# Optimization experiments

Hardware: AMD Instinct MI355X
Metric: run time of the kernel (lower is better)

The kernel has to match this reference:

```python
import jax, jax.numpy as jnp
import numpy as np

N_NODES = 100000


def sage_conv(x, src, dst, W_l, b_l, W_r):
    # PyG SAGEConv (aggr='mean'): out = lin_l(mean_{j->i} x_j) + lin_r(x_i)
    # lin_l has bias, lin_r does not.
    msgs = x[src]                                             # [E, d_in] irregular gather
    summed = jax.ops.segment_sum(msgs, dst, num_segments=N_NODES)
    deg = jax.ops.segment_sum(jnp.ones((src.shape[0],), x.dtype), dst,
                              num_segments=N_NODES)
    mean = summed / jnp.maximum(deg, 1.0)[:, None]            # [N, d_in]
    return mean @ W_l.T + b_l + x @ W_r.T                     # [N, d_out]


def setup_inputs() -> dict:
    key = jax.random.key(0)
    ks = jax.random.split(key, 8)
    input_dim, hidden_dim, output_dim = 64, 128, 64
    E = 1600000
    x = jax.random.normal(ks[0], (N_NODES, input_dim), dtype=jnp.float32)
    edge_index = jax.random.randint(ks[1], (2, E), 0, N_NODES, dtype=jnp.int64)

    def glorot(k, shape):
        lim = (6.0 / (shape[0] + shape[1])) ** 0.5
        return jax.random.uniform(k, shape, jnp.float32, -lim, lim)

    W1_l = glorot(ks[2], (hidden_dim, input_dim))
    b1 = jnp.zeros((hidden_dim,), jnp.float32)
    W1_r = glorot(ks[3], (hidden_dim, input_dim))
    W2_l = glorot(ks[4], (output_dim, hidden_dim))
    b2 = jnp.zeros((output_dim,), jnp.float32)
    W2_r = glorot(ks[5], (output_dim, hidden_dim))
    return {"x": x, "edge_index": edge_index,
            "W1_l": W1_l, "b1": b1, "W1_r": W1_r,
            "W2_l": W2_l, "b2": b2, "W2_r": W2_r}


def reference(x, edge_index, W1_l, b1, W1_r, W2_l, b2, W2_r):
    src, dst = edge_index[0], edge_index[1]
    h = jax.nn.relu(sage_conv(x, src, dst, W1_l, b1, W1_r))
    h = jax.nn.relu(sage_conv(h, src, dst, W2_l, b2, W2_r))
    # Original module computes norm(x) and dropout(x) but discards the results,
    # so the returned value is just the second ReLU output.
    return h
```

## Files before the change

kernel.cpp:

```cpp
#include <hip/hip_runtime.h>
#include <hip/hip_bf16.h>


#define NODE_DIM0 64
#define NPBK 256
#define MAXB 512
#define CAPB 5120
#define EPB  4096
#define NSL  16

__device__ inline unsigned short f2bf(float f) {
    unsigned u = __float_as_uint(f);
    return (unsigned short)((u + 0x7fffu + ((u >> 16) & 1u)) >> 16);
}


__global__ __launch_bounds__(256) void bucket_scatter(const int* __restrict__ src,
                                                      const int* __restrict__ dst,
                                                      int* __restrict__ gcur,
                                                      unsigned* __restrict__ pairs, int E) {
    __shared__ int hist[MAXB];
    __shared__ int incl[MAXB];
    __shared__ int exoff[MAXB];
    __shared__ int cur[MAXB];
    __shared__ int chunkBase[MAXB];
    __shared__ unsigned staged[EPB];
    __shared__ unsigned short sbkt[EPB];
    const int t = threadIdx.x;
    const int base = blockIdx.x * EPB;
    int cnt = E - base; if (cnt > EPB) cnt = EPB;

    hist[t] = 0; hist[t + 256] = 0;
    __syncthreads();

    int myS[16], myD[16];
#pragma unroll
    for (int it = 0; it < 16; ++it) {
        int e = base + it * 256 + t;
        if (e < E) {
            myS[it] = src[e];
            myD[it] = dst[e];
            atomicAdd(&hist[myD[it] >> 8], 1);
        } else {
            myD[it] = -1;
        }
    }
    __syncthreads();

    incl[t] = hist[t]; incl[t + 256] = hist[t + 256];
    __syncthreads();
    for (int o = 1; o < MAXB; o <<= 1) {
        int a0 = (t >= o) ? incl[t - o] : 0;
        int a1 = (t + 256 >= o) ? incl[t + 256 - o] : 0;
        __syncthreads();
        incl[t] += a0; incl[t + 256] += a1;
        __syncthreads();
    }
    exoff[t] = incl[t] - hist[t];
    exoff[t + 256] = incl[t + 256] - hist[t + 256];
    cur[t] = 0; cur[t + 256] = 0;
    chunkBase[t] = (hist[t] > 0) ? atomicAdd(&gcur[t], hist[t]) : 0;
    chunkBase[t + 256] = (hist[t + 256] > 0) ? atomicAdd(&gcur[t + 256], hist[t + 256]) : 0;
    __syncthreads();

#pragma unroll
    for (int it = 0; it < 16; ++it) {
        if (myD[it] >= 0) {
            int b = myD[it] >> 8;
            int p = exoff[b] + atomicAdd(&cur[b], 1);
            staged[p] = ((unsigned)(myD[it] & (NPBK - 1)) << 17) | (unsigned)myS[it];
            sbkt[p] = (unsigned short)b;
        }
    }
    __syncthreads();

    for (int p = t; p < cnt; p += 256) {
        int b = sbkt[p];
        int g = chunkBase[b] + (p - exoff[b]);
        if (g < CAPB) pairs[(size_t)b * CAPB + g] = staged[p];
    }
}


__global__ __launch_bounds__(256) void bucket_csr(const unsigned* __restrict__ pairs,
                                                  const int* __restrict__ gcur,
                                                  int* __restrict__ startA,
                                                  int* __restrict__ degA,
                                                  int* __restrict__ esrc, int N) {
    __shared__ int ldeg[NPBK * NSL];
    __shared__ int lcur[NPBK * NSL];
    __shared__ int lsrc[CAPB];
    __shared__ int wsum[256];
    const int b = blockIdx.x;
    const int t = threadIdx.x;
    int cnt = gcur[b]; if (cnt > CAPB) cnt = CAPB;

    for (int i = t; i < NPBK * NSL; i += 256) ldeg[i] = 0;
    __syncthreads();

    const unsigned* reg = pairs + (size_t)b * CAPB;
    for (int i = t; i < cnt; i += 256) {
        unsigned w = reg[i];
        atomicAdd(&ldeg[((w >> 17) << 4) | ((w & 0x1FFFFu) >> 13)], 1);
    }
    __syncthreads();

    const int base = t * NSL;
    int run = 0, loc[NSL];
#pragma unroll
    for (int k = 0; k < NSL; ++k) { loc[k] = run; run += ldeg[base + k]; }
    wsum[t] = run;
    __syncthreads();
    for (int o = 1; o < 256; o <<= 1) {
        int add = (t >= o) ? wsum[t - o] : 0;
        __syncthreads();
        wsum[t] += add;
        __syncthreads();
    }
    const int excl = wsum[t] - run;
#pragma unroll
    for (int k = 0; k < NSL; ++k) lcur[base + k] = excl + loc[k];
    const int node0 = b * NPBK;
    if (node0 + t < N) { startA[node0 + t] = b * CAPB + excl; degA[node0 + t] = run; }
    __syncthreads();

    for (int i = t; i < cnt; i += 256) {
        unsigned w = reg[i];
        int key = ((w >> 17) << 4) | ((w & 0x1FFFFu) >> 13);
        int pos = atomicAdd(&lcur[key], 1);
        lsrc[pos] = (int)(w & 0x1FFFFu);
    }
    __syncthreads();

    int* out = esrc + (size_t)b * CAPB;
    for (int i = t; i < cnt; i += 256) out[i] = lsrc[i];
}


__global__ void cast_bf(const float* __restrict__ in, unsigned short* __restrict__ out, int n4) {
    int i = blockIdx.x * 256 + threadIdx.x;
    if (i < n4) {
        float4 v = ((const float4*)in)[i];
        ushort4 o;
        o.x = f2bf(v.x); o.y = f2bf(v.y); o.z = f2bf(v.z); o.w = f2bf(v.w);
        ((ushort4*)out)[i] = o;
    }
}

__global__ void cast_weights(const float* __restrict__ a, const float* __restrict__ b,
                             const float* __restrict__ c, const float* __restrict__ d,
                             unsigned short* __restrict__ oa, unsigned short* __restrict__ ob,
                             unsigned short* __restrict__ oc, unsigned short* __restrict__ od) {
    int i = blockIdx.x * 256 + threadIdx.x;
    if (i < 8192) {
        oa[i] = f2bf(a[i]); ob[i] = f2bf(b[i]);
        oc[i] = f2bf(c[i]); od[i] = f2bf(d[i]);
    }
}


template <int MODE>
__global__ __launch_bounds__(256) void gather64(const unsigned short* __restrict__ feat,
                                                const int* __restrict__ startA,
                                                const int* __restrict__ degA,
                                                const int* __restrict__ esrc,
                                                const unsigned short* __restrict__ sdata,
                                                unsigned short* __restrict__ meanOut,
                                                float* __restrict__ outF, int n) {
    const int w = (blockIdx.x * 256 + threadIdx.x) >> 3;
    const int fl = threadIdx.x & 7;
    if (w >= n) return;
    const int s0 = startA[w], dg = degA[w];
    float acc[8] = {0.f, 0.f, 0.f, 0.f, 0.f, 0.f, 0.f, 0.f};
    const int* ep = esrc + s0;
    int e = 0;
    for (; e + 8 <= dg; e += 8) {
        int s_[8];
#pragma unroll
        for (int k = 0; k < 8; ++k) s_[k] = ep[e + k];
        uint4 u[8];
#pragma unroll
        for (int k = 0; k < 8; ++k)
            u[k] = *(const uint4*)(feat + (size_t)s_[k] * 64 + fl * 8);
#pragma unroll
        for (int k = 0; k < 8; ++k) {
            acc[0] += __uint_as_float(u[k].x << 16);
            acc[1] += __uint_as_float(u[k].x & 0xffff0000u);
            acc[2] += __uint_as_float(u[k].y << 16);
            acc[3] += __uint_as_float(u[k].y & 0xffff0000u);
            acc[4] += __uint_as_float(u[k].z << 16);
            acc[5] += __uint_as_float(u[k].z & 0xffff0000u);
            acc[6] += __uint_as_float(u[k].w << 16);
            acc[7] += __uint_as_float(u[k].w & 0xffff0000u);
        }
    }
    for (; e < dg; ++e) {
        uint4 u = *(const uint4*)(feat + (size_t)ep[e] * 64 + fl * 8);
        acc[0] += __uint_as_float(u.x << 16);
        acc[1] += __uint_as_float(u.x & 0xffff0000u);
        acc[2] += __uint_as_float(u.y << 16);
        acc[3] += __uint_as_float(u.y & 0xffff0000u);
        acc[4] += __uint_as_float(u.z << 16);
        acc[5] += __uint_as_float(u.z & 0xffff0000u);
        acc[6] += __uint_as_float(u.w << 16);
        acc[7] += __uint_as_float(u.w & 0xffff0000u);
    }
    const float inv = 1.0f / fmaxf((float)dg, 1.0f);
    if (MODE == 0) {
        unsigned us[8];
#pragma unroll
        for (int q = 0; q < 8; ++q) us[q] = f2bf(acc[q] * inv);
        uint4 o4;
        o4.x = us[0] | (us[1] << 16);
        o4.y = us[2] | (us[3] << 16);
        o4.z = us[4] | (us[5] << 16);
        o4.w = us[6] | (us[7] << 16);
        *(uint4*)(meanOut + (size_t)w * 64 + fl * 8) = o4;
    } else {
        uint4 us = *(const uint4*)(sdata + (size_t)w * 64 + fl * 8);
        float sv8[8];
        sv8[0] = __uint_as_float(us.x << 16);
        sv8[1] = __uint_as_float(us.x & 0xffff0000u);
        sv8[2] = __uint_as_float(us.y << 16);
        sv8[3] = __uint_as_float(us.y & 0xffff0000u);
        sv8[4] = __uint_as_float(us.z << 16);
        sv8[5] = __uint_as_float(us.z & 0xffff0000u);
        sv8[6] = __uint_as_float(us.w << 16);
        sv8[7] = __uint_as_float(us.w & 0xffff0000u);
        float4 o0, o1;
        o0.x = fmaxf(acc[0] * inv + sv8[0], 0.f);
        o0.y = fmaxf(acc[1] * inv + sv8[1], 0.f);
        o0.z = fmaxf(acc[2] * inv + sv8[2], 0.f);
        o0.w = fmaxf(acc[3] * inv + sv8[3], 0.f);
        o1.x = fmaxf(acc[4] * inv + sv8[4], 0.f);
        o1.y = fmaxf(acc[5] * inv + sv8[5], 0.f);
        o1.z = fmaxf(acc[6] * inv + sv8[6], 0.f);
        o1.w = fmaxf(acc[7] * inv + sv8[7], 0.f);
        *(float4*)(outF + (size_t)w * 64 + fl * 8)     = o0;
        *(float4*)(outF + (size_t)w * 64 + fl * 8 + 4) = o1;
    }
}


__global__ __launch_bounds__(256) void fused_l12(const unsigned short* __restrict__ meanb,
                                                 const unsigned short* __restrict__ selfb,
                                                 const unsigned short* __restrict__ W1l,
                                                 const float* __restrict__ b1,
                                                 const unsigned short* __restrict__ W1r,
                                                 const unsigned short* __restrict__ W2l,
                                                 const float* __restrict__ b2,
                                                 const unsigned short* __restrict__ W2r,
                                                 unsigned short* __restrict__ zout,
                                                 unsigned short* __restrict__ sout, int n) {
    using bf16x8 = __attribute__((ext_vector_type(8))) short;
    using f32x4  = __attribute__((ext_vector_type(4))) float;
    constexpr int LDW = 136;
    __shared__ unsigned short h1t[16 * LDW];
    const int wv   = threadIdx.x >> 6;
    const int lane = threadIdx.x & 63;
    const int row16 = lane & 15;
    const int quad  = lane >> 4;

    bf16x8 bl1[2][2], br1[2][2];
    float bv1[2];
#pragma unroll
    for (int r = 0; r < 2; ++r) {
        int nc = (wv * 2 + r) * 16 + row16;
#pragma unroll
        for (int kk = 0; kk < 2; ++kk) {
            bl1[r][kk] = *(const bf16x8*)(W1l + (size_t)nc * 64 + kk * 32 + quad * 8);
            br1[r][kk] = *(const bf16x8*)(W1r + (size_t)nc * 64 + kk * 32 + quad * 8);
        }
        bv1[r] = b1[nc];
    }
    const int nc2 = wv * 16 + row16;
    bf16x8 bl2[4], br2[4];
#pragma unroll
    for (int kk = 0; kk < 4; ++kk) {
        bl2[kk] = *(const bf16x8*)(W2l + (size_t)nc2 * 128 + kk * 32 + quad * 8);
        br2[kk] = *(const bf16x8*)(W2r + (size_t)nc2 * 128 + kk * 32 + quad * 8);
    }
    const float bv2 = b2[nc2];

    const int mtiles = n / 16;
    for (int mt = blockIdx.x; mt < mtiles; mt += gridDim.x) {
        const int m = mt * 16 + row16;
        bf16x8 am[2], as2[2];
#pragma unroll
        for (int kk = 0; kk < 2; ++kk) {
            am[kk]  = *(const bf16x8*)(meanb + (size_t)m * 64 + kk * 32 + quad * 8);
            as2[kk] = *(const bf16x8*)(selfb + (size_t)m * 64 + kk * 32 + quad * 8);
        }
#pragma unroll
        for (int r = 0; r < 2; ++r) {
            f32x4 acc = {0.f, 0.f, 0.f, 0.f};
#pragma unroll
            for (int kk = 0; kk < 2; ++kk)
                acc = __builtin_amdgcn_mfma_f32_16x16x32_bf16(am[kk], bl1[r][kk], acc, 0, 0, 0);
#pragma unroll
            for (int kk = 0; kk < 2; ++kk)
                acc = __builtin_amdgcn_mfma_f32_16x16x32_bf16(as2[kk], br1[r][kk], acc, 0, 0, 0);
            const int nc = (wv * 2 + r) * 16 + row16;
#pragma unroll
            for (int i = 0; i < 4; ++i)
                h1t[(quad * 4 + i) * LDW + nc] = f2bf(fmaxf(acc[i] + bv1[r], 0.f));
        }
        __syncthreads();
        bf16x8 a2[4];
#pragma unroll
        for (int kk = 0; kk < 4; ++kk)
            a2[kk] = *(const bf16x8*)(h1t + row16 * LDW + kk * 32 + quad * 8);
        f32x4 accz = {0.f, 0.f, 0.f, 0.f};
        f32x4 accs = {0.f, 0.f, 0.f, 0.f};
#pragma unroll
        for (int kk = 0; kk < 4; ++kk) {
            accz = __builtin_amdgcn_mfma_f32_16x16x32_bf16(a2[kk], bl2[kk], accz, 0, 0, 0);
            accs = __builtin_amdgcn_mfma_f32_16x16x32_bf16(a2[kk], br2[kk], accs, 0, 0, 0);
        }
        const int rowb = mt * 16 + quad * 4;
#pragma unroll
        for (int i = 0; i < 4; ++i) {
            zout[(size_t)(rowb + i) * 64 + nc2] = f2bf(accz[i]);
            sout[(size_t)(rowb + i) * 64 + nc2] = f2bf(accs[i] + bv2);
        }
        __syncthreads();
    }
}


static inline char* align_up(char* p, size_t a) {
    return (char*)(((uintptr_t)p + a - 1) & ~(uintptr_t)(a - 1));
}

extern "C" void kernel_launch(void* const* d_in, const int* in_sizes, int n_in,
                              void* d_out, int out_size, void* d_ws, size_t ws_size,
                              hipStream_t stream) {
    const float* x   = (const float*)d_in[0];
    const int*   ei  = (const int*)d_in[1];
    const float* W1l = (const float*)d_in[2];
    const float* b1  = (const float*)d_in[3];
    const float* W1r = (const float*)d_in[4];
    const float* W2l = (const float*)d_in[5];
    const float* b2  = (const float*)d_in[6];
    const float* W2r = (const float*)d_in[7];
    float* out = (float*)d_out;

    const int N = in_sizes[0] / NODE_DIM0;
    const int E = in_sizes[1] / 2;
    const int* src = ei;
    const int* dst = ei + E;
    const int nbuck = (N + NPBK - 1) / NPBK;

    char* p = (char*)d_ws;
    int* gcur   = (int*)p; p += (size_t)MAXB * 4;          p = align_up(p, 16);
    int* startA = (int*)p; p += (size_t)N * 4;             p = align_up(p, 16);
    int* degA   = (int*)p; p += (size_t)N * 4;             p = align_up(p, 16);
    int* esrc   = (int*)p; p += (size_t)nbuck * CAPB * 4;  p = align_up(p, 16);
    unsigned short* xbf   = (unsigned short*)p; p += (size_t)N * 64 * 2;
    unsigned short* scr2  = (unsigned short*)p; p += (size_t)N * 128 * 2;
    unsigned short* wl1bf = (unsigned short*)p; p += (size_t)128 * 64 * 2;
    unsigned short* wr1bf = (unsigned short*)p; p += (size_t)128 * 64 * 2;
    unsigned short* wl2bf = (unsigned short*)p; p += (size_t)64 * 128 * 2;
    unsigned short* wr2bf = (unsigned short*)p; p += (size_t)64 * 128 * 2;
    unsigned short* meanbf = (unsigned short*)p; p += (size_t)N * 64 * 2;

    unsigned* pairs = (unsigned*)scr2;
    unsigned short* zbf = scr2;
    unsigned short* sbf = scr2 + (size_t)N * 64;

    hipMemsetAsync(gcur, 0, (size_t)MAXB * 4, stream);
    bucket_scatter<<<(E + EPB - 1) / EPB, 256, 0, stream>>>(src, dst, gcur, pairs, E);
    bucket_csr<<<nbuck, 256, 0, stream>>>(pairs, gcur, startA, degA, esrc, N);

    cast_bf<<<(N * 64 / 4 + 255) / 256, 256, 0, stream>>>(x, xbf, N * 64 / 4);
    cast_weights<<<32, 256, 0, stream>>>(W1l, W1r, W2l, W2r, wl1bf, wr1bf, wl2bf, wr2bf);

    gather64<0><<<(N * 8 + 255) / 256, 256, 0, stream>>>(xbf, startA, degA, esrc, nullptr, meanbf, nullptr, N);

    fused_l12<<<1024, 256, 0, stream>>>(meanbf, xbf, wl1bf, b1, wr1bf,
                                        wl2bf, b2, wr2bf, zbf, sbf, N);

    gather64<1><<<(N * 8 + 255) / 256, 256, 0, stream>>>(zbf, startA, degA, esrc, sbf, nullptr, out, N);
}
```

Baseline: 224.5 us.

## Drop LDS staging in bucket build, fold memset and weight casts into kernels

The bucket scatter now uses the rank returned by its shared-memory histogram atomic to write pairs straight to global memory, which removes the prefix scan and the staged LDS copy. The CSR kernel likewise keeps each element's rank in registers and scatters directly into esrc without an LDS buffer. The gcur memset moves into the cast kernel, and the weight cast kernel is removed, with fused_l12 converting fp32 weights to bf16 as it loads them. This cuts two launches and several block barriers, but the global writes become less coalesced. Each of the 1024 fused blocks also repeats the weight conversion.

```diff
diff --git a/kernel.cpp b/kernel.cpp
--- a/kernel.cpp
+++ b/kernel.cpp
@@ -20,64 +20,41 @@
                                                       int* __restrict__ gcur,
                                                       unsigned* __restrict__ pairs, int E) {
     __shared__ int hist[MAXB];
-    __shared__ int incl[MAXB];
-    __shared__ int exoff[MAXB];
-    __shared__ int cur[MAXB];
     __shared__ int chunkBase[MAXB];
-    __shared__ unsigned staged[EPB];
-    __shared__ unsigned short sbkt[EPB];
     const int t = threadIdx.x;
     const int base = blockIdx.x * EPB;
-    int cnt = E - base; if (cnt > EPB) cnt = EPB;
 
     hist[t] = 0; hist[t + 256] = 0;
     __syncthreads();
 
-    int myS[16], myD[16];
+    int myS[16], myD[16], myR[16];
 #pragma unroll
     for (int it = 0; it < 16; ++it) {
         int e = base + it * 256 + t;
         if (e < E) {
             myS[it] = src[e];
             myD[it] = dst[e];
-            atomicAdd(&hist[myD[it] >> 8], 1);
+            myR[it] = atomicAdd(&hist[myD[it] >> 8], 1);
         } else {
             myD[it] = -1;
         }
     }
     __syncthreads();
 
-    incl[t] = hist[t]; incl[t + 256] = hist[t + 256];
-    __syncthreads();
-    for (int o = 1; o < MAXB; o <<= 1) {
-        int a0 = (t >= o) ? incl[t - o] : 0;
-        int a1 = (t + 256 >= o) ? incl[t + 256 - o] : 0;
-        __syncthreads();
-        incl[t] += a0; incl[t + 256] += a1;
-        __syncthreads();
-    }
-    exoff[t] = incl[t] - hist[t];
-    exoff[t + 256] = incl[t + 256] - hist[t + 256];
-    cur[t] = 0; cur[t + 256] = 0;
-    chunkBase[t] = (hist[t] > 0) ? atomicAdd(&gcur[t], hist[t]) : 0;
-    chunkBase[t + 256] = (hist[t + 256] > 0) ? atomicAdd(&gcur[t + 256], hist[t + 256]) : 0;
+    int h0 = hist[t], h1 = hist[t + 256];
+    chunkBase[t]       = (h0 > 0) ? atomicAdd(&gcur[t], h0) : 0;
+    chunkBase[t + 256] = (h1 > 0) ? atomicAdd(&gcur[t + 256], h1) : 0;
     __syncthreads();
 
 #pragma unroll
     for (int it = 0; it < 16; ++it) {
         if (myD[it] >= 0) {
             int b = myD[it] >> 8;
-            int p = exoff[b] + atomicAdd(&cur[b], 1);
-            staged[p] = ((unsigned)(myD[it] & (NPBK - 1)) << 17) | (unsigned)myS[it];
-            sbkt[p] = (unsigned short)b;
-        }
-    }
-    __syncthreads();
-
-    for (int p = t; p < cnt; p += 256) {
-        int b = sbkt[p];
-        int g = chunkBase[b] + (p - exoff[b]);
-        if (g < CAPB) pairs[(size_t)b * CAPB + g] = staged[p];
+            int g = chunkBase[b] + myR[it];
+            if (g < CAPB)
+                pairs[(size_t)b * CAPB + g] =
+                    ((unsigned)(myD[it] & (NPBK - 1)) << 17) | (unsigned)myS[it];
+        }
     }
 }
 
@@ -88,8 +65,7 @@
                                                   int* __restrict__ degA,
                                                   int* __restrict__ esrc, int N) {
     __shared__ int ldeg[NPBK * NSL];
-    __shared__ int lcur[NPBK * NSL];
-    __shared__ int lsrc[CAPB];
+    __shared__ int koff[NPBK * NSL];
     __shared__ int wsum[256];
     const int b = blockIdx.x;
     const int t = threadIdx.x;
@@ -99,16 +75,22 @@
     __syncthreads();
 
     const unsigned* reg = pairs + (size_t)b * CAPB;
+    unsigned myW[20]; int myR[20], myK[20];
+    int nn = 0;
     for (int i = t; i < cnt; i += 256) {
         unsigned w = reg[i];
-        atomicAdd(&ldeg[((w >> 17) << 4) | ((w & 0x1FFFFu) >> 13)], 1);
-    }
-    __syncthreads();
-
-    const int base = t * NSL;
+        int key = (int)((w >> 17) << 4) | (int)((w & 0x1FFFFu) >> 13);
+        myW[nn] = w;
+        myK[nn] = key;
+        myR[nn] = atomicAdd(&ldeg[key], 1);
+        ++nn;
+    }
+    __syncthreads();
+
+    const int kbase = t * NSL;
     int run = 0, loc[NSL];
 #pragma unroll
-    for (int k = 0; k < NSL; ++k) { loc[k] = run; run += ldeg[base + k]; }
+    for (int k = 0; k < NSL; ++k) { loc[k] = run; run += ldeg[kbase + k]; }
     wsum[t] = run;
     __syncthreads();
     for (int o = 1; o < 256; o <<= 1) {
@@ -119,42 +101,27 @@
     }
     const int excl = wsum[t] - run;
 #pragma unroll
-    for (int k = 0; k < NSL; ++k) lcur[base + k] = excl + loc[k];
+    for (int k = 0; k < NSL; ++k) koff[kbase + k] = excl + loc[k];
     const int node0 = b * NPBK;
     if (node0 + t < N) { startA[node0 + t] = b * CAPB + excl; degA[node0 + t] = run; }
     __syncthreads();
 
-    for (int i = t; i < cnt; i += 256) {
-        unsigned w = reg[i];
-        int key = ((w >> 17) << 4) | ((w & 0x1FFFFu) >> 13);
-        int pos = atomicAdd(&lcur[key], 1);
-        lsrc[pos] = (int)(w & 0x1FFFFu);
-    }
-    __syncthreads();
-
-    int* out = esrc + (size_t)b * CAPB;
-    for (int i = t; i < cnt; i += 256) out[i] = lsrc[i];
-}
-
-
-__global__ void cast_bf(const float* __restrict__ in, unsigned short* __restrict__ out, int n4) {
+    int* outp = esrc + (size_t)b * CAPB;
+    for (int k = 0; k < nn; ++k)
+        outp[koff[myK[k]] + myR[k]] = (int)(myW[k] & 0x1FFFFu);
+}
+
+
+__global__ void cast_bf(const float* __restrict__ in, unsigned short* __restrict__ out,
+                        int n4, int* __restrict__ gcur) {
+    if (blockIdx.x == 0)
+        for (int j = threadIdx.x; j < MAXB; j += 256) gcur[j] = 0;
     int i = blockIdx.x * 256 + threadIdx.x;
     if (i < n4) {
         float4 v = ((const float4*)in)[i];
         ushort4 o;
         o.x = f2bf(v.x); o.y = f2bf(v.y); o.z = f2bf(v.z); o.w = f2bf(v.w);
         ((ushort4*)out)[i] = o;
-    }
-}
-
-__global__ void cast_weights(const float* __restrict__ a, const float* __restrict__ b,
-                             const float* __restrict__ c, const float* __restrict__ d,
-                             unsigned short* __restrict__ oa, unsigned short* __restrict__ ob,
-                             unsigned short* __restrict__ oc, unsigned short* __restrict__ od) {
-    int i = blockIdx.x * 256 + threadIdx.x;
-    if (i < 8192) {
-        oa[i] = f2bf(a[i]); ob[i] = f2bf(b[i]);
-        oc[i] = f2bf(c[i]); od[i] = f2bf(d[i]);
     }
 }
 
@@ -244,12 +211,12 @@
 
 __global__ __launch_bounds__(256) void fused_l12(const unsigned short* __restrict__ meanb,
                                                  const unsigned short* __restrict__ selfb,
-                                                 const unsigned short* __restrict__ W1l,
+                                                 const float* __restrict__ W1l,
                                                  const float* __restrict__ b1,
-                                                 const unsigned short* __restrict__ W1r,
-                                                 const unsigned short* __restrict__ W2l,
+                                                 const float* __restrict__ W1r,
+                                                 const float* __restrict__ W2l,
                                                  const float* __restrict__ b2,
-                                                 const unsigned short* __restrict__ W2r,
+                                                 const float* __restrict__ W2r,
                                                  unsigned short* __restrict__ zout,
                                                  unsigned short* __restrict__ sout, int n) {
     using bf16x8 = __attribute__((ext_vector_type(8))) short;
@@ -268,8 +235,13 @@
         int nc = (wv * 2 + r) * 16 + row16;
 #pragma unroll
         for (int kk = 0; kk < 2; ++kk) {
-            bl1[r][kk] = *(const bf16x8*)(W1l + (size_t)nc * 64 + kk * 32 + quad * 8);
-            br1[r][kk] = *(const bf16x8*)(W1r + (size_t)nc * 64 + kk * 32 + quad * 8);
+            const float* pl = W1l + (size_t)nc * 64 + kk * 32 + quad * 8;
+            const float* pr = W1r + (size_t)nc * 64 + kk * 32 + quad * 8;
+#pragma unroll
+            for (int i = 0; i < 8; ++i) {
+                bl1[r][kk][i] = (short)f2bf(pl[i]);
+                br1[r][kk][i] = (short)f2bf(pr[i]);
+            }
         }
         bv1[r] = b1[nc];
     }
@@ -277,8 +249,13 @@
     bf16x8 bl2[4], br2[4];
 #pragma unroll
     for (int kk = 0; kk < 4; ++kk) {
-        bl2[kk] = *(const bf16x8*)(W2l + (size_t)nc2 * 128 + kk * 32 + quad * 8);
-        br2[kk] = *(const bf16x8*)(W2r + (size_t)nc2 * 128 + kk * 32 + quad * 8);
+        const float* pl = W2l + (size_t)nc2 * 128 + kk * 32 + quad * 8;
+        const float* pr = W2r + (size_t)nc2 * 128 + kk * 32 + quad * 8;
+#pragma unroll
+        for (int i = 0; i < 8; ++i) {
+            bl2[kk][i] = (short)f2bf(pl[i]);
+            br2[kk][i] = (short)f2bf(pr[i]);
+        }
     }
     const float bv2 = b2[nc2];
 
@@ -358,27 +335,21 @@
     int* esrc   = (int*)p; p += (size_t)nbuck * CAPB * 4;  p = align_up(p, 16);
     unsigned short* xbf   = (unsigned short*)p; p += (size_t)N * 64 * 2;
     unsigned short* scr2  = (unsigned short*)p; p += (size_t)N * 128 * 2;
-    unsigned short* wl1bf = (unsigned short*)p; p += (size_t)128 * 64 * 2;
-    unsigned short* wr1bf = (unsigned short*)p; p += (size_t)128 * 64 * 2;
-    unsigned short* wl2bf = (unsigned short*)p; p += (size_t)64 * 128 * 2;
-    unsigned short* wr2bf = (unsigned short*)p; p += (size_t)64 * 128 * 2;
     unsigned short* meanbf = (unsigned short*)p; p += (size_t)N * 64 * 2;
 
     unsigned* pairs = (unsigned*)scr2;
     unsigned short* zbf = scr2;
     unsigned short* sbf = scr2 + (size_t)N * 64;
 
-    hipMemsetAsync(gcur, 0, (size_t)MAXB * 4, stream);
+    cast_bf<<<(N * 64 / 4 + 255) / 256, 256, 0, stream>>>(x, xbf, N * 64 / 4, gcur);
+
     bucket_scatter<<<(E + EPB - 1) / EPB, 256, 0, stream>>>(src, dst, gcur, pairs, E);
     bucket_csr<<<nbuck, 256, 0, stream>>>(pairs, gcur, startA, degA, esrc, N);
 
-    cast_bf<<<(N * 64 / 4 + 255) / 256, 256, 0, stream>>>(x, xbf, N * 64 / 4);
-    cast_weights<<<32, 256, 0, stream>>>(W1l, W1r, W2l, W2r, wl1bf, wr1bf, wl2bf, wr2bf);
-
     gather64<0><<<(N * 8 + 255) / 256, 256, 0, stream>>>(xbf, startA, degA, esrc, nullptr, meanbf, nullptr, N);
 
-    fused_l12<<<1024, 256, 0, stream>>>(meanbf, xbf, wl1bf, b1, wr1bf,
-                                        wl2bf, b2, wr2bf, zbf, sbf, N);
+    fused_l12<<<1024, 256, 0, stream>>>(meanbf, xbf, W1l, b1, W1r,
+                                        W2l, b2, W2r, zbf, sbf, N);
 
     gather64<1><<<(N * 8 + 255) / 256, 256, 0, stream>>>(zbf, startA, degA, esrc, sbf, nullptr, out, N);
 }
```

After: 240.0 us. 6.9% more time.
